# Optimization experiments

Hardware: AMD Instinct MI355X
Metric: run time of the kernel (lower is better)

## Reference

```python
import jax, jax.numpy as jnp
import numpy as np

ALPHA = 0.2          # LeakyReLU negative slope
NEG_INF = -9e15      # mask fill value used by the original module


def setup_inputs() -> dict:
    key = jax.random.key(0)
    k1, k2, k3, k4 = jax.random.split(key, 4)
    N, F_in, F_out = 8192, 256, 64
    h = jax.random.normal(k1, (N, F_in), dtype=jnp.float32)
    adj = jax.random.randint(k2, (N, N), 0, 2).astype(jnp.int32)
    # xavier_uniform with gain=1.414
    gain = 1.414
    bW = gain * np.sqrt(6.0 / (F_in + F_out))
    W = jax.random.uniform(k3, (F_in, F_out), dtype=jnp.float32, minval=-bW, maxval=bW)
    ba = gain * np.sqrt(6.0 / (2 * F_out + 1))
    a = jax.random.uniform(k4, (2 * F_out, 1), dtype=jnp.float32, minval=-ba, maxval=ba)
    return {"h": h, "adj": adj, "W": W, "a": a}


def reference(h, adj, W, a):
    # Wh: [N, F_out]
    Wh = h @ W
    F_out = Wh.shape[1]
    # Decompose a_input @ a: e[i, j] = leakyrelu(Wh[j]@a[:F] + Wh[i]@a[F:])
    # (repeat gives Wh[j] in the first half, repeat_interleave gives Wh[i] in the second)
    f_src = (Wh @ a[:F_out]).reshape(-1)   # [N], coefficient of column index j
    f_dst = (Wh @ a[F_out:]).reshape(-1)   # [N], coefficient of row index i
    e = jax.nn.leaky_relu(f_dst[:, None] + f_src[None, :], negative_slope=ALPHA)  # [N, N]
    attention = jnp.where(adj > 0, e, NEG_INF)
    attention = jax.nn.softmax(attention, axis=1)
    # dropout is identity in eval mode (training=False)
    h_prime = attention @ Wh               # [N, F_out]
    return jax.nn.elu(h_prime)             # concat=True path
```

## Files before the change

### kernel.cpp

```cpp
#include <hip/hip_runtime.h>
#include <hip/hip_bf16.h>

#define GN   8192
#define FIN  256
#define FOUT 64
#define SEGJ 1024
#define NSEG 8

typedef float  f32x4  __attribute__((ext_vector_type(4)));
typedef __bf16 bf16x8 __attribute__((ext_vector_type(8)));
typedef int    iv4    __attribute__((ext_vector_type(4)));

__device__ __forceinline__ unsigned short f2bf_rtne(float x) {
    unsigned int u = __float_as_uint(x);
    unsigned int r = (u + 0x7FFFu + ((u >> 16) & 1u)) >> 16;
    return (unsigned short)r;
}

__global__ __launch_bounds__(256) void k_wh(const float* __restrict__ h,
                                            const float* __restrict__ W,
                                            const float* __restrict__ a,
                                            float* __restrict__ fsrc,
                                            float* __restrict__ fdst,
                                            uint4* __restrict__ whfrag) {
    __shared__ float Wt[FOUT][FIN + 1];
    __shared__ float WhL[32][FOUT + 1];
    int t = threadIdx.x;
    int col = t & 63, kq4 = t >> 6;
#pragma unroll
    for (int rep = 0; rep < 16; ++rep) {
        int k0 = kq4 * 4 + rep * 16;
        float4 wv;
        wv.x = W[(k0 + 0) * FOUT + col];
        wv.y = W[(k0 + 1) * FOUT + col];
        wv.z = W[(k0 + 2) * FOUT + col];
        wv.w = W[(k0 + 3) * FOUT + col];
        *(float4*)&Wt[col][k0] = wv;
    }
    __syncthreads();
    int wave = t >> 6, lane = t & 63;
    float a1 = a[lane], a2 = a[FOUT + lane];
    int bid = blockIdx.x;
#pragma unroll
    for (int rr = 0; rr < 8; ++rr) {
        int il = wave * 8 + rr;
        int i  = bid * 32 + il;
        const float* hrow = h + (size_t)i * FIN;
        float acc = 0.f;
#pragma unroll 8
        for (int k0 = 0; k0 < FIN; k0 += 4) {
            float4 hv = *(const float4*)&hrow[k0];
            float4 wv = *(const float4*)&Wt[lane][k0];
            acc += hv.x * wv.x + hv.y * wv.y + hv.z * wv.z + hv.w * wv.w;
        }
        WhL[il][lane] = acc;
        float v1 = acc * a1, v2 = acc * a2;
#pragma unroll
        for (int off = 32; off > 0; off >>= 1) {
            v1 += __shfl_xor(v1, off);
            v2 += __shfl_xor(v2, off);
        }
        if (lane == 0) { fsrc[i] = fminf(v1, 30.f); fdst[i] = fminf(v2, 30.f); }
    }
    __syncthreads();
    int lane2 = t & 63, ct = t >> 6;
    int colc = ct * 16 + (lane2 & 15);
    int rbase = (lane2 >> 4) * 8;
    unsigned int pk[4];
#pragma unroll
    for (int p = 0; p < 4; ++p) {
        unsigned int lo = f2bf_rtne(WhL[rbase + 2 * p    ][colc]);
        unsigned int hi = f2bf_rtne(WhL[rbase + 2 * p + 1][colc]);
        pk[p] = lo | (hi << 16);
    }
    uint4 o; o.x = pk[0]; o.y = pk[1]; o.z = pk[2]; o.w = pk[3];
    whfrag[(size_t)(bid * 4 + ct) * 64 + lane2] = o;
}

__device__ __forceinline__ void produce_seg(const int* __restrict__ adj, int rowbase, int S,
                                            unsigned* __restrict__ bbuf, int wv, int lane) {
    const int* base = adj + (size_t)rowbase * GN + (size_t)S * SEGJ;
    iv4 st[32];
#pragma unroll
    for (int k = 0; k < 32; ++k) {
        int u = wv * 32 + k;
        st[k] = __builtin_nontemporal_load(
            (const iv4*)(base + (size_t)(u >> 2) * GN + (u & 3) * 256 + lane * 4));
    }
#pragma unroll
    for (int k = 0; k < 32; ++k) {
        int u = wv * 32 + k, row = u >> 2, Q = u & 3;
        unsigned long long b0 = __ballot(st[k][0] > 0);
        unsigned long long b1 = __ballot(st[k][1] > 0);
        unsigned long long b2 = __ballot(st[k][2] > 0);
        unsigned long long b3 = __ballot(st[k][3] > 0);
        if (lane < 8) {
            int c = lane >> 1, hh = lane & 1;
            unsigned long long bs = (c == 0) ? b0 : (c == 1) ? b1 : (c == 2) ? b2 : b3;
            bbuf[(Q * 8 + lane) * 33 + row] = (unsigned)(bs >> (hh * 32));
        }
    }
}

__global__ __launch_bounds__(512, 2) void k_fused(const int* __restrict__ adj,
                                                  const float* __restrict__ fsrc,
                                                  const float* __restrict__ fdst,
                                                  const uint4* __restrict__ whfrag,
                                                  float* __restrict__ out) {
    __shared__ unsigned bitsS[2][1056];
    __shared__ __align__(16) float redS[4][64][20];
    __shared__ float denS[2][2][16];
    int t = threadIdx.x, wv = t >> 6, lane = t & 63;
    int rowbase = blockIdx.x * 32;

    f32x4 acc0 = {0.f, 0.f, 0.f, 0.f}, acc1 = acc0, acc2 = acc0, acc3 = acc0;
    float den = 0.f;
    int m = (wv - 4) >> 1, p = (wv - 4) & 1;
    int r = lane & 15, g = lane >> 4;
    float d = 0.f;
    if (wv >= 4) d = fdst[rowbase + m * 16 + r];

    if (wv < 4) produce_seg(adj, rowbase, 0, bitsS[0], wv, lane);
    __syncthreads();

    for (int S = 0; S < NSEG; ++S) {
        if (wv < 4) {
            if (S + 1 < NSEG) produce_seg(adj, rowbase, S + 1, bitsS[(S + 1) & 1], wv, lane);
        } else {
            const unsigned* bbuf = bitsS[S & 1];
            int jb0 = S * 32;
            int ch = p;
            const uint4* bp = whfrag + (size_t)(jb0 + ch) * 256 + lane;
            uint4 b0 = bp[0], b1 = bp[64], b2 = bp[128], b3 = bp[192];
            const float* sp = fsrc + S * SEGJ + ch * 32 + g * 8;
            float4 s0 = *(const float4*)sp, s1 = *(const float4*)(sp + 4);
            int row = m * 16 + r;
#pragma unroll 4
            for (int k = 0; k < 16; ++k) {
                int chn = (k < 15) ? ch + 2 : ch;
                const uint4* bpn = whfrag + (size_t)(jb0 + chn) * 256 + lane;
                uint4 nb0 = bpn[0], nb1 = bpn[64], nb2 = bpn[128], nb3 = bpn[192];
                const float* spn = fsrc + S * SEGJ + chn * 32 + g * 8;
                float4 ns0 = *(const float4*)spn, ns1 = *(const float4*)(spn + 4);

                int Q = ch >> 3, hh = (ch >> 2) & 1, sh = (ch & 3) * 8 + g * 2;
                int wb = (Q * 8 + hh) * 33 + row;
                unsigned wcs[4] = {bbuf[wb], bbuf[wb + 66], bbuf[wb + 132], bbuf[wb + 198]};

                float se[8] = {s0.x, s0.y, s0.z, s0.w, s1.x, s1.y, s1.z, s1.w};
                bf16x8 af;
                float ws = 0.f;
#pragma unroll
                for (int e = 0; e < 8; ++e) {
                    float ev = d + se[e];
                    float lr = fmaxf(ev, 0.2f * ev);
                    float ex = __expf(lr);
                    unsigned bit = (wcs[e & 3] >> (sh + (e >> 2))) & 1u;
                    float wvv = bit ? ex : 0.f;
                    ws += wvv;
                    af[e] = (__bf16)wvv;
                }
                den += ws;
                acc0 = __builtin_amdgcn_mfma_f32_16x16x32_bf16(af, __builtin_bit_cast(bf16x8, b0), acc0, 0, 0, 0);
                acc1 = __builtin_amdgcn_mfma_f32_16x16x32_bf16(af, __builtin_bit_cast(bf16x8, b1), acc1, 0, 0, 0);
                acc2 = __builtin_amdgcn_mfma_f32_16x16x32_bf16(af, __builtin_bit_cast(bf16x8, b2), acc2, 0, 0, 0);
                acc3 = __builtin_amdgcn_mfma_f32_16x16x32_bf16(af, __builtin_bit_cast(bf16x8, b3), acc3, 0, 0, 0);
                ch = chn; b0 = nb0; b1 = nb1; b2 = nb2; b3 = nb3; s0 = ns0; s1 = ns1;
            }
        }
        __syncthreads();
    }

    if (wv >= 4) {
        int cw = wv - 4;
        *(f32x4*)&redS[cw][lane][0]  = acc0;
        *(f32x4*)&redS[cw][lane][4]  = acc1;
        *(f32x4*)&redS[cw][lane][8]  = acc2;
        *(f32x4*)&redS[cw][lane][12] = acc3;
        den += __shfl_xor(den, 16);
        den += __shfl_xor(den, 32);
        if (lane < 16) denS[m][p][lane] = den;
    }
    __syncthreads();

    {
        int row = t >> 4;
        int c0  = (t & 15) * 4;
        int mm = row >> 4, q = (row >> 2) & 3, reg = row & 3;
        float dd = denS[mm][0][row & 15] + denS[mm][1][row & 15];
        float inv = (dd != 0.f) ? 1.f / dd : 0.f;
        float4 o;
        float* op = &o.x;
#pragma unroll
        for (int cc = 0; cc < 4; ++cc) {
            int col = c0 + cc;
            int l   = q * 16 + (col & 15);
            int idx = (col >> 4) * 4 + reg;
            float num = redS[mm * 2 + 0][l][idx] + redS[mm * 2 + 1][l][idx];
            float v = num * inv;
            op[cc] = v > 0.f ? v : __expf(v) - 1.f;
        }
        *(float4*)&out[(size_t)(rowbase + row) * FOUT + c0] = o;
    }
}

extern "C" void kernel_launch(void* const* d_in, const int* in_sizes, int n_in,
                              void* d_out, int out_size, void* d_ws, size_t ws_size,
                              hipStream_t stream) {
    (void)in_sizes; (void)n_in; (void)out_size; (void)ws_size;
    const float* h   = (const float*)d_in[0];
    const int*   adj = (const int*)d_in[1];
    const float* W   = (const float*)d_in[2];
    const float* a   = (const float*)d_in[3];
    float* out = (float*)d_out;

    float* ws     = (float*)d_ws;
    float* fsrc   = ws;
    float* fdst   = ws + GN;
    uint4* whfrag = (uint4*)(ws + 2 * GN);

    k_wh   <<<GN / 32, 256, 0, stream>>>(h, W, a, fsrc, fdst, whfrag);
    k_fused<<<GN / 32, 512, 0, stream>>>(adj, fsrc, fdst, whfrag, out);
}
```

Measured before the change: 119.1 us.

## Split attention over column segments with partial sums and separate reduction kernel

```diff
diff --git a/kernel.cpp b/kernel.cpp
--- a/kernel.cpp
+++ b/kernel.cpp
@@ -1,11 +1,15 @@
 #include <hip/hip_runtime.h>
 #include <hip/hip_bf16.h>
 
-#define GN   8192
-#define FIN  256
-#define FOUT 64
-#define SEGJ 1024
-#define NSEG 8
+#define GN     8192
+#define FIN    256
+#define FOUT   64
+#define NSPLIT 8
+#define JSEG   1024
+#define NCH    32
+#define PF     4
+#define ROWS_B 128
+#define LOG2E  1.44269504f
 
 typedef float  f32x4  __attribute__((ext_vector_type(4)));
 typedef __bf16 bf16x8 __attribute__((ext_vector_type(8)));
@@ -60,7 +64,10 @@
             v1 += __shfl_xor(v1, off);
             v2 += __shfl_xor(v2, off);
         }
-        if (lane == 0) { fsrc[i] = fminf(v1, 30.f); fdst[i] = fminf(v2, 30.f); }
+        if (lane == 0) {
+            fsrc[i] = fminf(v1, 30.f) * LOG2E;
+            fdst[i] = fminf(v2, 30.f) * LOG2E;
+        }
     }
     __syncthreads();
     int lane2 = t & 63, ct = t >> 6;
@@ -77,131 +84,109 @@
     whfrag[(size_t)(bid * 4 + ct) * 64 + lane2] = o;
 }
 
-__device__ __forceinline__ void produce_seg(const int* __restrict__ adj, int rowbase, int S,
-                                            unsigned* __restrict__ bbuf, int wv, int lane) {
-    const int* base = adj + (size_t)rowbase * GN + (size_t)S * SEGJ;
-    iv4 st[32];
-#pragma unroll
-    for (int k = 0; k < 32; ++k) {
-        int u = wv * 32 + k;
-        st[k] = __builtin_nontemporal_load(
-            (const iv4*)(base + (size_t)(u >> 2) * GN + (u & 3) * 256 + lane * 4));
-    }
-#pragma unroll
-    for (int k = 0; k < 32; ++k) {
-        int u = wv * 32 + k, row = u >> 2, Q = u & 3;
-        unsigned long long b0 = __ballot(st[k][0] > 0);
-        unsigned long long b1 = __ballot(st[k][1] > 0);
-        unsigned long long b2 = __ballot(st[k][2] > 0);
-        unsigned long long b3 = __ballot(st[k][3] > 0);
-        if (lane < 8) {
-            int c = lane >> 1, hh = lane & 1;
-            unsigned long long bs = (c == 0) ? b0 : (c == 1) ? b1 : (c == 2) ? b2 : b3;
-            bbuf[(Q * 8 + lane) * 33 + row] = (unsigned)(bs >> (hh * 32));
-        }
-    }
-}
-
-__global__ __launch_bounds__(512, 2) void k_fused(const int* __restrict__ adj,
-                                                  const float* __restrict__ fsrc,
-                                                  const float* __restrict__ fdst,
-                                                  const uint4* __restrict__ whfrag,
-                                                  float* __restrict__ out) {
-    __shared__ unsigned bitsS[2][1056];
-    __shared__ __align__(16) float redS[4][64][20];
-    __shared__ float denS[2][2][16];
+__global__ __launch_bounds__(512, 2) void k_attn(const int* __restrict__ adj,
+                                                 const float* __restrict__ fsrc,
+                                                 const float* __restrict__ fdst,
+                                                 const uint4* __restrict__ whfrag,
+                                                 float* __restrict__ pacc,
+                                                 float* __restrict__ pden) {
+    __shared__ uint4 whL[NCH * 4 * 64];
+    __shared__ float fsL[JSEG];
+
     int t = threadIdx.x, wv = t >> 6, lane = t & 63;
-    int rowbase = blockIdx.x * 32;
+    int bid = blockIdx.x;
+    int rt = bid >> 3, q = bid & (NSPLIT - 1);
+    int rowbase = rt * ROWS_B;
+
+    {
+        const uint4* src = whfrag + (size_t)q * (NCH * 4 * 64);
+#pragma unroll
+        for (int it = 0; it < 16; ++it) whL[it * 512 + t] = src[it * 512 + t];
+        if (t < 256) *(float4*)&fsL[t * 4] = *(const float4*)&fsrc[q * JSEG + t * 4];
+    }
+    __syncthreads();
+
+    int r = lane & 15, g = lane >> 4;
+    int row = rowbase + wv * 16 + r;
+    float d = fdst[row];
+    const int* arow = adj + (size_t)row * GN + q * JSEG + g * 8;
 
     f32x4 acc0 = {0.f, 0.f, 0.f, 0.f}, acc1 = acc0, acc2 = acc0, acc3 = acc0;
     float den = 0.f;
-    int m = (wv - 4) >> 1, p = (wv - 4) & 1;
-    int r = lane & 15, g = lane >> 4;
-    float d = 0.f;
-    if (wv >= 4) d = fdst[rowbase + m * 16 + r];
-
-    if (wv < 4) produce_seg(adj, rowbase, 0, bitsS[0], wv, lane);
-    __syncthreads();
-
-    for (int S = 0; S < NSEG; ++S) {
-        if (wv < 4) {
-            if (S + 1 < NSEG) produce_seg(adj, rowbase, S + 1, bitsS[(S + 1) & 1], wv, lane);
-        } else {
-            const unsigned* bbuf = bitsS[S & 1];
-            int jb0 = S * 32;
-            int ch = p;
-            const uint4* bp = whfrag + (size_t)(jb0 + ch) * 256 + lane;
-            uint4 b0 = bp[0], b1 = bp[64], b2 = bp[128], b3 = bp[192];
-            const float* sp = fsrc + S * SEGJ + ch * 32 + g * 8;
-            float4 s0 = *(const float4*)sp, s1 = *(const float4*)(sp + 4);
-            int row = m * 16 + r;
-#pragma unroll 4
-            for (int k = 0; k < 16; ++k) {
-                int chn = (k < 15) ? ch + 2 : ch;
-                const uint4* bpn = whfrag + (size_t)(jb0 + chn) * 256 + lane;
-                uint4 nb0 = bpn[0], nb1 = bpn[64], nb2 = bpn[128], nb3 = bpn[192];
-                const float* spn = fsrc + S * SEGJ + chn * 32 + g * 8;
-                float4 ns0 = *(const float4*)spn, ns1 = *(const float4*)(spn + 4);
-
-                int Q = ch >> 3, hh = (ch >> 2) & 1, sh = (ch & 3) * 8 + g * 2;
-                int wb = (Q * 8 + hh) * 33 + row;
-                unsigned wcs[4] = {bbuf[wb], bbuf[wb + 66], bbuf[wb + 132], bbuf[wb + 198]};
-
-                float se[8] = {s0.x, s0.y, s0.z, s0.w, s1.x, s1.y, s1.z, s1.w};
-                bf16x8 af;
-                float ws = 0.f;
-#pragma unroll
-                for (int e = 0; e < 8; ++e) {
-                    float ev = d + se[e];
-                    float lr = fmaxf(ev, 0.2f * ev);
-                    float ex = __expf(lr);
-                    unsigned bit = (wcs[e & 3] >> (sh + (e >> 2))) & 1u;
-                    float wvv = bit ? ex : 0.f;
-                    ws += wvv;
-                    af[e] = (__bf16)wvv;
-                }
-                den += ws;
-                acc0 = __builtin_amdgcn_mfma_f32_16x16x32_bf16(af, __builtin_bit_cast(bf16x8, b0), acc0, 0, 0, 0);
-                acc1 = __builtin_amdgcn_mfma_f32_16x16x32_bf16(af, __builtin_bit_cast(bf16x8, b1), acc1, 0, 0, 0);
-                acc2 = __builtin_amdgcn_mfma_f32_16x16x32_bf16(af, __builtin_bit_cast(bf16x8, b2), acc2, 0, 0, 0);
-                acc3 = __builtin_amdgcn_mfma_f32_16x16x32_bf16(af, __builtin_bit_cast(bf16x8, b3), acc3, 0, 0, 0);
-                ch = chn; b0 = nb0; b1 = nb1; b2 = nb2; b3 = nb3; s0 = ns0; s1 = ns1;
+
+    iv4 pfa[PF], pfb[PF];
+#pragma unroll
+    for (int dd = 0; dd < PF; ++dd) {
+        pfa[dd] = __builtin_nontemporal_load((const iv4*)(arow + dd * 32));
+        pfb[dd] = __builtin_nontemporal_load((const iv4*)(arow + dd * 32 + 4));
+    }
+
+    for (int cb = 0; cb < NCH; cb += PF) {
+#pragma unroll
+        for (int dd = 0; dd < PF; ++dd) {
+            int ch = cb + dd;
+            int ae[8] = {pfa[dd][0], pfa[dd][1], pfa[dd][2], pfa[dd][3],
+                         pfb[dd][0], pfb[dd][1], pfb[dd][2], pfb[dd][3]};
+            float4 s0 = *(const float4*)&fsL[ch * 32 + g * 8];
+            float4 s1 = *(const float4*)&fsL[ch * 32 + g * 8 + 4];
+            float se[8] = {s0.x, s0.y, s0.z, s0.w, s1.x, s1.y, s1.z, s1.w};
+
+            int nch = ch + PF;
+            if (nch < NCH) {
+                pfa[dd] = __builtin_nontemporal_load((const iv4*)(arow + nch * 32));
+                pfb[dd] = __builtin_nontemporal_load((const iv4*)(arow + nch * 32 + 4));
             }
-        }
-        __syncthreads();
-    }
-
-    if (wv >= 4) {
-        int cw = wv - 4;
-        *(f32x4*)&redS[cw][lane][0]  = acc0;
-        *(f32x4*)&redS[cw][lane][4]  = acc1;
-        *(f32x4*)&redS[cw][lane][8]  = acc2;
-        *(f32x4*)&redS[cw][lane][12] = acc3;
-        den += __shfl_xor(den, 16);
-        den += __shfl_xor(den, 32);
-        if (lane < 16) denS[m][p][lane] = den;
-    }
-    __syncthreads();
-
-    {
-        int row = t >> 4;
-        int c0  = (t & 15) * 4;
-        int mm = row >> 4, q = (row >> 2) & 3, reg = row & 3;
-        float dd = denS[mm][0][row & 15] + denS[mm][1][row & 15];
-        float inv = (dd != 0.f) ? 1.f / dd : 0.f;
-        float4 o;
-        float* op = &o.x;
-#pragma unroll
-        for (int cc = 0; cc < 4; ++cc) {
-            int col = c0 + cc;
-            int l   = q * 16 + (col & 15);
-            int idx = (col >> 4) * 4 + reg;
-            float num = redS[mm * 2 + 0][l][idx] + redS[mm * 2 + 1][l][idx];
-            float v = num * inv;
-            op[cc] = v > 0.f ? v : __expf(v) - 1.f;
-        }
-        *(float4*)&out[(size_t)(rowbase + row) * FOUT + c0] = o;
-    }
+
+            bf16x8 af;
+            float ws = 0.f;
+#pragma unroll
+            for (int e = 0; e < 8; ++e) {
+                float ev = d + se[e];
+                float lr = fmaxf(ev, 0.2f * ev);
+                float ex = __builtin_amdgcn_exp2f(lr);
+                float wvv = (ae[e] > 0) ? ex : 0.f;
+                ws += wvv;
+                af[e] = (__bf16)wvv;
+            }
+            den += ws;
+
+            const uint4* bl = &whL[(ch * 4) * 64 + lane];
+            uint4 b0 = bl[0], b1 = bl[64], b2 = bl[128], b3 = bl[192];
+            acc0 = __builtin_amdgcn_mfma_f32_16x16x32_bf16(af, __builtin_bit_cast(bf16x8, b0), acc0, 0, 0, 0);
+            acc1 = __builtin_amdgcn_mfma_f32_16x16x32_bf16(af, __builtin_bit_cast(bf16x8, b1), acc1, 0, 0, 0);
+            acc2 = __builtin_amdgcn_mfma_f32_16x16x32_bf16(af, __builtin_bit_cast(bf16x8, b2), acc2, 0, 0, 0);
+            acc3 = __builtin_amdgcn_mfma_f32_16x16x32_bf16(af, __builtin_bit_cast(bf16x8, b3), acc3, 0, 0, 0);
+        }
+    }
+
+    den += __shfl_xor(den, 16);
+    den += __shfl_xor(den, 32);
+
+    float* po = pacc + (size_t)q * (GN * FOUT);
+    int orow = rowbase + wv * 16 + g * 4;
+#pragma unroll
+    for (int reg = 0; reg < 4; ++reg) {
+        po[(size_t)(orow + reg) * FOUT +  0 + r] = acc0[reg];
+        po[(size_t)(orow + reg) * FOUT + 16 + r] = acc1[reg];
+        po[(size_t)(orow + reg) * FOUT + 32 + r] = acc2[reg];
+        po[(size_t)(orow + reg) * FOUT + 48 + r] = acc3[reg];
+    }
+    if (g == 0) pden[(size_t)q * GN + row] = den;
+}
+
+__global__ __launch_bounds__(256) void k_out(const float* __restrict__ pacc,
+                                             const float* __restrict__ pden,
+                                             float* __restrict__ out) {
+    int idx = blockIdx.x * 256 + threadIdx.x;
+    int i = idx >> 6;
+    float num = 0.f, den = 0.f;
+#pragma unroll
+    for (int qq = 0; qq < NSPLIT; ++qq) {
+        num += pacc[(size_t)qq * (GN * FOUT) + idx];
+        den += pden[(size_t)qq * GN + i];
+    }
+    float v = (den != 0.f) ? num / den : 0.f;
+    out[idx] = v > 0.f ? v : __expf(v) - 1.f;
 }
 
 extern "C" void kernel_launch(void* const* d_in, const int* in_sizes, int n_in,
@@ -216,9 +201,12 @@
 
     float* ws     = (float*)d_ws;
     float* fsrc   = ws;
-    float* fdst   = ws + GN;
-    uint4* whfrag = (uint4*)(ws + 2 * GN);
-
-    k_wh   <<<GN / 32, 256, 0, stream>>>(h, W, a, fsrc, fdst, whfrag);
-    k_fused<<<GN / 32, 512, 0, stream>>>(adj, fsrc, fdst, whfrag, out);
-}
+    float* fdst   = fsrc + GN;
+    uint4* whfrag = (uint4*)(fdst + GN);
+    float* pacc   = (float*)(whfrag + (size_t)GN / 32 * 4 * 64);
+    float* pden   = pacc + (size_t)NSPLIT * GN * FOUT;
+
+    k_wh  <<<GN / 32,                    256, 0, stream>>>(h, W, a, fsrc, fdst, whfrag);
+    k_attn<<<(GN / ROWS_B) * NSPLIT,     512, 0, stream>>>(adj, fsrc, fdst, whfrag, pacc, pden);
+    k_out <<<GN * FOUT / 256,            256, 0, stream>>>(pacc, pden, out);
+}
```

Result: faster. 113.1 us (-5.1%).
